# Kernel optimization log

Hardware: AMD Instinct MI355X
Metric: run time of the kernel (lower is better)

The kernel has to match this reference:

```python
import jax, jax.numpy as jnp
import numpy as np

B, T, H, F, Z = 4096, 16, 256, 256, 128   # batch, time_step, hidden, feature_dims, z_dims
P, PREV = 10, 5                           # predicted_visit, previous_visit


def _dense(x, W, b):
    return jax.nn.relu(x @ W + b)


def _forward(h_i, input_t, noise_post, noise_prior, W_lstm, U_lstm, b_lstm,
             W1, b1, W2, b2, W3, b3, W4, b4, W5, b5, W6, b6, W7, b7, W8, b8, W9, b9,
             alpha, beta, base):
    batch = h_i.shape[0]
    c = jnp.zeros((batch, H), h_i.dtype)
    h = jnp.zeros((batch, H), h_i.dtype)
    z_j = jnp.zeros((batch, Z), h_i.dtype)
    y_prev = jnp.zeros((batch, F), h_i.dtype)
    ys, m_post, lv_post, m_prior, lv_prior, z_post, z_prior, probs = ([] for _ in range(8))
    for j in range(P):  # sequential decode loop (true recurrence)
        cti = PREV + j
        # --- Hawkes intensity over growing history window [0, cti) ---
        ct = input_t[:, cti:cti + 1]                 # [B,1] current event time
        tb = input_t[:, :cti]                        # [B,cti] times before t
        tk = jnp.sum(jnp.exp(beta * (tb - ct)), axis=1, keepdims=True)   # [B,1]
        lam = base + alpha * tk                      # conditional intensity [B,1]
        last = input_t[:, cti - 1:cti]               # [B,1]
        td3 = jnp.sum(jnp.exp(beta * (tb - last)), axis=1, keepdims=True)
        prob = lam * jnp.exp((last - ct) * base + (alpha / beta) * (tk - td3))  # [B,1]
        # --- LSTM cell step (keras gate order i,f,c,o) ---
        x = jnp.concatenate([z_j, h_i, y_prev], axis=1)   # [B, Z+H+F]
        gates = x @ W_lstm + h @ U_lstm + b_lstm
        gi, gf, gg, go = jnp.split(gates, 4, axis=1)
        c = jax.nn.sigmoid(gf) * c + jax.nn.sigmoid(gi) * jnp.tanh(gg)
        h_raw = jax.nn.sigmoid(go) * jnp.tanh(c)          # LSTM output == new hidden
        h = lam * h_raw                                   # Hawkes-modulated hidden carried forward
        # --- emission ---
        y = _dense(_dense(_dense(h_raw, W1, b1), W2, b2), W3, b3)
        # --- inference (posterior) network ---
        hz = _dense(jnp.concatenate([h_i, h_raw, y, y_prev], axis=1), W4, b4)
        mean_j = _dense(hz, W5, b5)
        logv_j = _dense(hz, W6, b6)
        zj = mean_j + noise_post[j] * jnp.sqrt(jnp.exp(logv_j))
        # --- prior network ---
        hz_p = _dense(jnp.concatenate([h_i, h_raw, y_prev], axis=1), W7, b7)
        mean_p = _dense(hz_p, W8, b8)
        logv_p = _dense(hz_p, W9, b9)
        zp = mean_p + noise_prior[j] * jnp.sqrt(jnp.exp(logv_p))
        ys.append(y); m_post.append(mean_j); lv_post.append(logv_j)
        m_prior.append(mean_p); lv_prior.append(logv_p)
        z_post.append(zj); z_prior.append(zp); probs.append(prob)
        z_j, y_prev = zj, y
    return (jnp.stack(ys, 1),        # fake_input       [B,P,F]
            jnp.stack(m_post, 1),    # mean_all_post    [B,P,Z]
            jnp.stack(lv_post, 1),   # log_var_all_post [B,P,Z]
            jnp.stack(m_prior, 1),   # mean_all_prior   [B,P,Z]
            jnp.stack(lv_prior, 1),  # log_var_all_prior[B,P,Z]
            jnp.stack(z_post, 0),    # posterior z_all  [P,B,Z]
            jnp.stack(z_prior, 0),   # prior z_all      [P,B,Z]
            jnp.concatenate(probs, 0))  # time probs [P*B,1]


def setup_inputs() -> dict:
    key = jax.random.key(0)
    ks = jax.random.split(key, 20)
    u = lambda k, shape: jax.random.uniform(k, shape, jnp.float32, -0.05, 0.05)
    in_dim = Z + H + F
    return {
        "h_i": jax.random.normal(ks[0], (B, H), jnp.float32),
        "input_t": jnp.cumsum(jax.random.uniform(ks[1], (B, T), jnp.float32), axis=1),  # increasing event times
        "noise_post": jax.random.normal(ks[2], (P, B, Z), jnp.float32),
        "noise_prior": jax.random.normal(ks[3], (P, B, Z), jnp.float32),
        "W_lstm": u(ks[4], (in_dim, 4 * H)),
        "U_lstm": u(ks[5], (H, 4 * H)),
        "b_lstm": jnp.zeros((4 * H,), jnp.float32),
        "W1": u(ks[6], (H, F)), "b1": jnp.zeros((F,), jnp.float32),
        "W2": u(ks[7], (F, F)), "b2": jnp.zeros((F,), jnp.float32),
        "W3": u(ks[8], (F, F)), "b3": jnp.zeros((F,), jnp.float32),
        "W4": u(ks[9], (2 * H + 2 * F, Z)), "b4": jnp.zeros((Z,), jnp.float32),
        "W5": u(ks[10], (Z, Z)), "b5": jnp.zeros((Z,), jnp.float32),
        "W6": u(ks[11], (Z, Z)), "b6": jnp.zeros((Z,), jnp.float32),
        "W7": u(ks[12], (2 * H + F, Z)), "b7": jnp.zeros((Z,), jnp.float32),
        "W8": u(ks[13], (Z, Z)), "b8": jnp.zeros((Z,), jnp.float32),
        "W9": u(ks[14], (Z, Z)), "b9": jnp.zeros((Z,), jnp.float32),
        "alpha": u(ks[15], (1, 1)),
        "beta": u(ks[16], (1, 1)) + 0.1,   # keep away from 0 (alpha/beta division)
        "base": u(ks[17], (1, 1)),
    }


def reference(h_i, input_t, noise_post, noise_prior, W_lstm, U_lstm, b_lstm,
              W1, b1, W2, b2, W3, b3, W4, b4, W5, b5, W6, b6, W7, b7, W8, b8, W9, b9,
              alpha, beta, base):
    return _forward(h_i, input_t, noise_post, noise_prior, W_lstm, U_lstm, b_lstm,
                    W1, b1, W2, b2, W3, b3, W4, b4, W5, b5, W6, b6, W7, b7, W8, b8, W9, b9,
                    alpha, beta, base)
```

## Files before the change

### kernel.cpp

```cpp
#include <hip/hip_runtime.h>
#include <hip/hip_bf16.h>
#include <cstdint>
#include <cstddef>

#define DEVI __device__ __forceinline__

typedef __bf16 v8bf __attribute__((ext_vector_type(8)));
typedef float  v4f  __attribute__((ext_vector_type(4)));
using u16 = unsigned short;

constexpr int kB = 4096, kT = 16, kH = 256, kF = 256, kZ = 128, kP = 10, kPrev = 5;
constexpr int kRows = 16;
constexpr int kThreads = 1024;

constexpr size_t OFF_WzT = 0;
constexpr size_t OFF_WhT = OFF_WzT + (size_t)1024 * 128;
constexpr size_t OFF_WyT = OFF_WhT + (size_t)1024 * 256;
constexpr size_t OFF_UT  = OFF_WyT + (size_t)1024 * 256;
constexpr size_t OFF_W1T = OFF_UT  + (size_t)1024 * 256;
constexpr size_t OFF_W2T = OFF_W1T + (size_t)256 * 256;
constexpr size_t OFF_W3T = OFF_W2T + (size_t)256 * 256;
constexpr size_t OFF_W4T = OFF_W3T + (size_t)256 * 256;
constexpr size_t OFF_W5T = OFF_W4T + (size_t)128 * 1024;
constexpr size_t OFF_W6T = OFF_W5T + (size_t)128 * 128;
constexpr size_t OFF_W7T = OFF_W6T + (size_t)128 * 128;
constexpr size_t OFF_W8T = OFF_W7T + (size_t)128 * 768;
constexpr size_t OFF_W9T = OFF_W8T + (size_t)128 * 128;
constexpr size_t OFF_WEND= OFF_W9T + (size_t)128 * 128;

constexpr size_t O_YS   = 0;
constexpr size_t O_MPO  = O_YS   + (size_t)kB * kP * kF;
constexpr size_t O_LVPO = O_MPO  + (size_t)kB * kP * kZ;
constexpr size_t O_MPR  = O_LVPO + (size_t)kB * kP * kZ;
constexpr size_t O_LVPR = O_MPR  + (size_t)kB * kP * kZ;
constexpr size_t O_ZPO  = O_LVPR + (size_t)kB * kP * kZ;
constexpr size_t O_ZPR  = O_ZPO  + (size_t)kP * kB * kZ;
constexpr size_t O_PROB = O_ZPR  + (size_t)kP * kB * kZ;

DEVI float bf2f(u16 u) { return __uint_as_float(((unsigned)u) << 16); }
DEVI u16 f2bf(float f) {
    unsigned x = __float_as_uint(f);
    return (u16)((x + 0x7fffu + ((x >> 16) & 1u)) >> 16);
}
DEVI unsigned pk2(float lo, float hi) { return (unsigned)f2bf(lo) | ((unsigned)f2bf(hi) << 16); }
DEVI float upk(unsigned u, int hi) { return __uint_as_float(hi ? (u & 0xffff0000u) : (u << 16)); }
DEVI float sigf(float x) { x = fminf(fmaxf(x, -40.f), 40.f); return 1.f / (1.f + __expf(-x)); }
DEVI float tanhf_(float x) {
    x = fminf(fmaxf(x, -15.f), 15.f);
    float e = __expf(2.f * x);
    return (e - 1.f) / (e + 1.f);
}
DEVI v8bf ld8(const u16* p) { return *(const v8bf*)p; }
DEVI void nts(float v, float* p) { __builtin_nontemporal_store(v, p); }
DEVI float ntl(const float* p) { return __builtin_nontemporal_load(p); }

template <int NTL>
DEVI void zacc(v4f (&a)[NTL]) {
#pragma unroll
    for (int t = 0; t < NTL; ++t) a[t] = v4f{0, 0, 0, 0};
}

template <int K, int NTL, class NFN>
DEVI void gemm_acc(v4f (&acc)[NTL], const u16* A, int astr,
                   const u16* __restrict__ WT, int wtK, int wtOff,
                   NFN nf, int ln, int q) {
    const u16* A0 = A + ln * astr + q * 8;
    const u16* B0 = WT + (size_t)ln * wtK + (size_t)wtOff + q * 8;
#pragma unroll
    for (int k0 = 0; k0 < K; k0 += 32) {
        v8bf b[NTL];
#pragma unroll
        for (int t = 0; t < NTL; ++t)
            b[t] = ld8(B0 + (size_t)nf(t) * wtK + k0);
        v8bf a0 = ld8(A0 + k0);
#pragma unroll
        for (int t = 0; t < NTL; ++t)
            acc[t] = __builtin_amdgcn_mfma_f32_16x16x32_bf16(a0, b[t], acc[t], 0, 0, 0);
    }
}

DEVI void gemm2_128(v4f& aA, v4f& aB, const u16* A, int astr,
                    const u16* __restrict__ BA, const u16* __restrict__ BB,
                    int ln, int q) {
    const u16* A0 = A + ln * astr + q * 8;
    const u16* pa = BA + (size_t)ln * 128 + q * 8;
    const u16* pb = BB + (size_t)ln * 128 + q * 8;
#pragma unroll
    for (int k0 = 0; k0 < 128; k0 += 32) {
        v8bf b1 = ld8(pa + k0);
        v8bf b2 = ld8(pb + k0);
        v8bf av = ld8(A0 + k0);
        aA = __builtin_amdgcn_mfma_f32_16x16x32_bf16(av, b1, aA, 0, 0, 0);
        aB = __builtin_amdgcn_mfma_f32_16x16x32_bf16(av, b2, aB, 0, 0, 0);
    }
}

template <int NTL, class NFN>
DEVI void epi_relu(v4f (&acc)[NTL], const float (&bias)[NTL],
                   u16* s_dst, int dstr, NFN nf, int ln, int q) {
#pragma unroll
    for (int t = 0; t < NTL; ++t)
#pragma unroll
        for (int r = 0; r < 4; ++r) {
            int rl = q * 4 + r, n = nf(t) + ln;
            s_dst[rl * dstr + n] = f2bf(fmaxf(acc[t][r] + bias[t], 0.f));
        }
}

__global__ void transpose_w(const float* __restrict__ Wl, const float* __restrict__ U,
                            const float* __restrict__ W1, const float* __restrict__ W2,
                            const float* __restrict__ W3, const float* __restrict__ W4,
                            const float* __restrict__ W5, const float* __restrict__ W6,
                            const float* __restrict__ W7, const float* __restrict__ W8,
                            const float* __restrict__ W9, u16* __restrict__ ws) {
    size_t e = (size_t)blockIdx.x * blockDim.x + threadIdx.x;
    auto tp = [&](size_t eo, size_t dst, const float* src, int K, int srcN, int rowOff) {
        size_t n = eo / (size_t)K;
        size_t k = eo - n * (size_t)K;
        ws[dst + eo] = f2bf(src[(size_t)(rowOff + k) * srcN + n]);
    };
    if      (e < OFF_WhT) tp(e - OFF_WzT, OFF_WzT, Wl, 128, 1024, 0);
    else if (e < OFF_WyT) tp(e - OFF_WhT, OFF_WhT, Wl, 256, 1024, 128);
    else if (e < OFF_UT)  tp(e - OFF_WyT, OFF_WyT, Wl, 256, 1024, 384);
    else if (e < OFF_W1T) tp(e - OFF_UT,  OFF_UT,  U,  256, 1024, 0);
    else if (e < OFF_W2T) tp(e - OFF_W1T, OFF_W1T, W1, 256, 256, 0);
    else if (e < OFF_W3T) tp(e - OFF_W2T, OFF_W2T, W2, 256, 256, 0);
    else if (e < OFF_W4T) tp(e - OFF_W3T, OFF_W3T, W3, 256, 256, 0);
    else if (e < OFF_W5T) tp(e - OFF_W4T, OFF_W4T, W4, 1024, 128, 0);
    else if (e < OFF_W6T) tp(e - OFF_W5T, OFF_W5T, W5, 128, 128, 0);
    else if (e < OFF_W7T) tp(e - OFF_W6T, OFF_W6T, W6, 128, 128, 0);
    else if (e < OFF_W8T) tp(e - OFF_W7T, OFF_W7T, W7, 768, 128, 0);
    else if (e < OFF_W9T) tp(e - OFF_W8T, OFF_W8T, W8, 128, 128, 0);
    else if (e < OFF_WEND)tp(e - OFF_W9T, OFF_W9T, W9, 128, 128, 0);
}

__global__ __launch_bounds__(1024, 1) void fused_vrnn(
    const float* __restrict__ g_hi, const float* __restrict__ g_t,
    const float* __restrict__ g_npo, const float* __restrict__ g_npr,
    const float* __restrict__ b_lstm, const float* __restrict__ b1,
    const float* __restrict__ b2, const float* __restrict__ b3,
    const float* __restrict__ b4, const float* __restrict__ b5,
    const float* __restrict__ b6, const float* __restrict__ b7,
    const float* __restrict__ b8, const float* __restrict__ b9,
    const float* __restrict__ g_alpha, const float* __restrict__ g_beta,
    const float* __restrict__ g_base,
    const u16* __restrict__ ws, float* __restrict__ out) {
    __shared__ __align__(16) u16 s_h[kRows][kH + 8];
    __shared__ __align__(16) u16 s_zj[kRows][kZ + 8];
    __shared__ __align__(16) u16 s_yp[2][kRows][kF + 8];
    __shared__ __align__(16) u16 s_hraw[kRows][kH + 8];
    __shared__ __align__(16) u16 s_t1[kRows][kF + 8];
    __shared__ __align__(16) u16 s_t2[kRows][kF + 8];
    __shared__ __align__(16) u16 s_hz[kRows][kZ + 8];
    __shared__ __align__(16) u16 s_hzp[kRows][kZ + 8];
    __shared__ float s_lam[kP][kRows];

    const int tid = threadIdx.x;
    const int w = tid >> 6, lane = tid & 63, ln = lane & 15, q = lane >> 4;
    const int wl = w & 7;
    const bool lo = (w < 8);
    const int r0 = blockIdx.x * kRows;

    for (int i = tid; i < kRows * (kH + 8); i += kThreads) (&s_h[0][0])[i] = 0;
    for (int i = tid; i < kRows * (kZ + 8); i += kThreads) (&s_zj[0][0])[i] = 0;
    for (int i = tid; i < 2 * kRows * (kF + 8); i += kThreads) (&s_yp[0][0][0])[i] = 0;
    for (int i = tid; i < kRows * kH; i += kThreads) {
        int r = i >> 8, c = i & (kH - 1);
        s_hraw[r][c] = f2bf(g_hi[(size_t)(r0 + r) * kH + c]);
    }

    if (tid < kRows) {
        const float alpha = g_alpha[0], beta = g_beta[0], base = g_base[0];
        float tv[kT];
#pragma unroll
        for (int i = 0; i < kT; ++i) tv[i] = g_t[(size_t)(r0 + tid) * kT + i];
#pragma unroll 1
        for (int j = 0; j < kP; ++j) {
            int cti = kPrev + j;
            float ct = tv[cti], last = tv[cti - 1];
            float tk = 0.f, td3 = 0.f;
            for (int i = 0; i < cti; ++i) {
                tk += __expf(beta * (tv[i] - ct));
                td3 += __expf(beta * (tv[i] - last));
            }
            float lam = base + alpha * tk;
            float prob = lam * __expf((last - ct) * base + (alpha / beta) * (tk - td3));
            s_lam[j][tid] = lam;
            nts(prob, &out[O_PROB + (size_t)j * kB + (size_t)(r0 + tid)]);
        }
    }

    auto nfg  = [&](int t) { return (t << 8) + (w << 4); };
    auto nf12 = [&](int t) { return (w + (t << 3)) << 4; };
    auto nf3  = [&](int)   { return w << 4; };
    auto nfh  = [&](int)   { return wl << 4; };

    float rbl[4];
#pragma unroll
    for (int g = 0; g < 4; ++g) rbl[g] = b_lstm[(g << 8) + (w << 4) + ln];
    float rb1[2] = {0.f, 0.f}, rb2[2] = {0.f, 0.f};
    if (lo) {
#pragma unroll
        for (int t = 0; t < 2; ++t) {
            rb1[t] = b1[nf12(t) + ln];
            rb2[t] = b2[nf12(t) + ln];
        }
    }
    const float rb3v = b3[(w << 4) + ln];
    const int nhl = (wl << 4) + ln;
    float rb4 = 0.f, rb5 = 0.f, rb6 = 0.f, rb7 = 0.f, rb8 = 0.f, rb9 = 0.f;
    if (lo) { rb5 = b5[nhl]; rb6 = b6[nhl]; }
    else    { rb4 = b4[nhl]; rb7 = b7[nhl]; rb8 = b8[nhl]; rb9 = b9[nhl]; }

    __syncthreads();

    unsigned ghi_p[4][2];
    unsigned h4i_p[2] = {0, 0};
    unsigned h7i_p[2] = {0, 0};
    {
        v4f acc[4]; zacc(acc);
        gemm_acc<256, 4>(acc, &s_hraw[0][0], kH + 8, ws + OFF_WhT, 256, 0, nfg, ln, q);
#pragma unroll
        for (int t = 0; t < 4; ++t) {
            ghi_p[t][0] = pk2(acc[t][0], acc[t][1]);
            ghi_p[t][1] = pk2(acc[t][2], acc[t][3]);
        }
    }
    if (!lo) {
        v4f a[1]; zacc(a);
        gemm_acc<256, 1>(a, &s_hraw[0][0], kH + 8, ws + OFF_W4T, 1024, 0, nfh, ln, q);
        h4i_p[0] = pk2(a[0][0], a[0][1]);
        h4i_p[1] = pk2(a[0][2], a[0][3]);
        v4f b[1]; zacc(b);
        gemm_acc<256, 1>(b, &s_hraw[0][0], kH + 8, ws + OFF_W7T, 768, 0, nfh, ln, q);
        h7i_p[0] = pk2(b[0][0], b[0][1]);
        h7i_p[1] = pk2(b[0][2], b[0][3]);
    }
    __syncthreads();

    float c_st[4] = {0.f, 0.f, 0.f, 0.f};

#pragma unroll 1
    for (int j = 0; j < kP; ++j) {
        const int cur = j & 1, nxt = cur ^ 1;

        {
            v4f acc[4]; zacc(acc);
            gemm_acc<128, 4>(acc, &s_zj[0][0], kZ + 8, ws + OFF_WzT, 128, 0, nfg, ln, q);
            gemm_acc<256, 4>(acc, &s_yp[cur][0][0], kF + 8, ws + OFF_WyT, 256, 0, nfg, ln, q);
            gemm_acc<256, 4>(acc, &s_h[0][0], kH + 8, ws + OFF_UT, 256, 0, nfg, ln, q);
            __syncthreads();
            const int nc = (w << 4) + ln;
#pragma unroll
            for (int r = 0; r < 4; ++r) {
                const int rl = q * 4 + r;
                float gi = acc[0][r] + upk(ghi_p[0][r >> 1], r & 1) + rbl[0];
                float gf = acc[1][r] + upk(ghi_p[1][r >> 1], r & 1) + rbl[1];
                float gg = acc[2][r] + upk(ghi_p[2][r >> 1], r & 1) + rbl[2];
                float go = acc[3][r] + upk(ghi_p[3][r >> 1], r & 1) + rbl[3];
                float cs = c_st[r];
                cs = sigf(gf) * cs + sigf(gi) * tanhf_(gg);
                float hr = sigf(go) * tanhf_(cs);
                c_st[r] = cs;
                float lamv = s_lam[j][rl];
                s_hraw[rl][nc] = f2bf(hr);
                s_h[rl][nc] = f2bf(lamv * hr);
            }
        }
        __syncthreads();

        v4f a4[1]; zacc(a4);

        if (lo) {
            v4f a1[2]; zacc(a1);
            gemm_acc<256, 2>(a1, &s_hraw[0][0], kH + 8, ws + OFF_W1T, 256, 0, nf12, ln, q);
            epi_relu<2>(a1, rb1, &s_t1[0][0], kF + 8, nf12, ln, q);
        } else {
            v4f a7[1]; zacc(a7);
            gemm_acc<256, 1>(a7, &s_hraw[0][0], kH + 8, ws + OFF_W7T, 768, 256, nfh, ln, q);
            gemm_acc<256, 1>(a7, &s_yp[cur][0][0], kF + 8, ws + OFF_W7T, 768, 512, nfh, ln, q);
#pragma unroll
            for (int r = 0; r < 4; ++r) {
                float v = a7[0][r] + upk(h7i_p[r >> 1], r & 1) + rb7;
                s_hzp[q * 4 + r][nhl] = f2bf(fmaxf(v, 0.f));
            }
        }
        __syncthreads();

        if (lo) {
            v4f a2[2]; zacc(a2);
            gemm_acc<256, 2>(a2, &s_t1[0][0], kF + 8, ws + OFF_W2T, 256, 0, nf12, ln, q);
            epi_relu<2>(a2, rb2, &s_t2[0][0], kF + 8, nf12, ln, q);
        } else {
            gemm_acc<256, 1>(a4, &s_hraw[0][0], kH + 8, ws + OFF_W4T, 1024, 256, nfh, ln, q);
            gemm_acc<256, 1>(a4, &s_yp[cur][0][0], kF + 8, ws + OFF_W4T, 1024, 768, nfh, ln, q);
        }
        __syncthreads();

        {
            v4f a3[1]; zacc(a3);
            v4f a8 = v4f{0, 0, 0, 0}, a9 = v4f{0, 0, 0, 0};
            gemm_acc<256, 1>(a3, &s_t2[0][0], kF + 8, ws + OFF_W3T, 256, 0, nf3, ln, q);
            if (!lo)
                gemm2_128(a8, a9, &s_hzp[0][0], kZ + 8,
                          ws + OFF_W8T + (size_t)(wl << 4) * 128,
                          ws + OFF_W9T + (size_t)(wl << 4) * 128, ln, q);
            const int n3 = (w << 4) + ln;
#pragma unroll
            for (int r = 0; r < 4; ++r) {
                int rl = q * 4 + r;
                size_t grow = (size_t)(r0 + rl);
                float yv = fmaxf(a3[0][r] + rb3v, 0.f);
                s_yp[nxt][rl][n3] = f2bf(yv);
                nts(yv, &out[O_YS + (grow * kP + j) * kF + n3]);
            }
            if (!lo) {
#pragma unroll
                for (int r = 0; r < 4; ++r) {
                    int rl = q * 4 + r;
                    size_t grow = (size_t)(r0 + rl);
                    float mp = fmaxf(a8[r] + rb8, 0.f);
                    float lp = fmaxf(a9[r] + rb9, 0.f);
                    nts(mp, &out[O_MPR + (grow * kP + j) * kZ + nhl]);
                    nts(lp, &out[O_LVPR + (grow * kP + j) * kZ + nhl]);
                    float nz = ntl(&g_npr[((size_t)j * kB + grow) * kZ + nhl]);
                    nts(mp + nz * __expf(0.5f * lp),
                        &out[O_ZPR + ((size_t)j * kB + grow) * kZ + nhl]);
                }
            }
        }
        __syncthreads();

        if (!lo) {
            gemm_acc<256, 1>(a4, &s_yp[nxt][0][0], kF + 8, ws + OFF_W4T, 1024, 512, nfh, ln, q);
#pragma unroll
            for (int r = 0; r < 4; ++r) {
                float v = a4[0][r] + upk(h4i_p[r >> 1], r & 1) + rb4;
                s_hz[q * 4 + r][nhl] = f2bf(fmaxf(v, 0.f));
            }
        }
        __syncthreads();

        if (lo) {
            v4f a5 = v4f{0, 0, 0, 0}, a6 = v4f{0, 0, 0, 0};
            gemm2_128(a5, a6, &s_hz[0][0], kZ + 8,
                      ws + OFF_W5T + (size_t)(w << 4) * 128,
                      ws + OFF_W6T + (size_t)(w << 4) * 128, ln, q);
#pragma unroll
            for (int r = 0; r < 4; ++r) {
                int rl = q * 4 + r;
                size_t grow = (size_t)(r0 + rl);
                float mn = fmaxf(a5[r] + rb5, 0.f);
                float lv = fmaxf(a6[r] + rb6, 0.f);
                nts(mn, &out[O_MPO + (grow * kP + j) * kZ + nhl]);
                nts(lv, &out[O_LVPO + (grow * kP + j) * kZ + nhl]);
                float nz = ntl(&g_npo[((size_t)j * kB + grow) * kZ + nhl]);
                float zj = mn + nz * __expf(0.5f * lv);
                s_zj[rl][nhl] = f2bf(zj);
                nts(zj, &out[O_ZPO + ((size_t)j * kB + grow) * kZ + nhl]);
            }
        }
        __syncthreads();
    }
}

extern "C" void kernel_launch(void* const* d_in, const int* in_sizes, int n_in,
                              void* d_out, int out_size, void* d_ws, size_t ws_size,
                              hipStream_t stream) {
    const float* hi  = (const float*)d_in[0];
    const float* it  = (const float*)d_in[1];
    const float* npo = (const float*)d_in[2];
    const float* npr = (const float*)d_in[3];
    const float* Wl  = (const float*)d_in[4];
    const float* U   = (const float*)d_in[5];
    const float* bl  = (const float*)d_in[6];
    const float* W1  = (const float*)d_in[7];
    const float* b1  = (const float*)d_in[8];
    const float* W2  = (const float*)d_in[9];
    const float* b2  = (const float*)d_in[10];
    const float* W3  = (const float*)d_in[11];
    const float* b3  = (const float*)d_in[12];
    const float* W4  = (const float*)d_in[13];
    const float* b4  = (const float*)d_in[14];
    const float* W5  = (const float*)d_in[15];
    const float* b5  = (const float*)d_in[16];
    const float* W6  = (const float*)d_in[17];
    const float* b6  = (const float*)d_in[18];
    const float* W7  = (const float*)d_in[19];
    const float* b7  = (const float*)d_in[20];
    const float* W8  = (const float*)d_in[21];
    const float* b8  = (const float*)d_in[22];
    const float* W9  = (const float*)d_in[23];
    const float* b9  = (const float*)d_in[24];
    const float* al  = (const float*)d_in[25];
    const float* be  = (const float*)d_in[26];
    const float* ba  = (const float*)d_in[27];
    u16* ws   = (u16*)d_ws;
    float* out = (float*)d_out;

    const unsigned tblocks = (unsigned)((OFF_WEND + 255) / 256);
    transpose_w<<<dim3(tblocks), dim3(256), 0, stream>>>(Wl, U, W1, W2, W3, W4, W5, W6, W7, W8, W9, ws);
    fused_vrnn<<<dim3(kB / kRows), dim3(kThreads), 0, stream>>>(
        hi, it, npo, npr, bl, b1, b2, b3, b4, b5, b6, b7, b8, b9, al, be, ba, ws, out);
}
```

Baseline: 1.373 ms.

## Pre-swizzle weights into MFMA fragment order for contiguous per-wave loads

The weight transpose kernel now writes each bf16 weight matrix in 16x32 MFMA B-fragment blocks, so every wave's lane reads 8 contiguous elements and one whole fragment is a contiguous 1 KB chunk. The gemm helpers index by tile and k-block instead of strided rows, which turns scattered row-strided global loads into fully coalesced ones. The launch bounds also change from a minimum of one block per CU to amdgpu_waves_per_eu(4,4), which alters the register budget the compiler is given. Fragment indexing must match the MFMA operand layout exactly or the results will be wrong.

```diff
diff --git a/kernel.cpp b/kernel.cpp
--- a/kernel.cpp
+++ b/kernel.cpp
@@ -60,19 +60,19 @@
     for (int t = 0; t < NTL; ++t) a[t] = v4f{0, 0, 0, 0};
 }
 
-template <int K, int NTL, class NFN>
+template <int KB, int NTL, class TFN>
 DEVI void gemm_acc(v4f (&acc)[NTL], const u16* A, int astr,
-                   const u16* __restrict__ WT, int wtK, int wtOff,
-                   NFN nf, int ln, int q) {
+                   const u16* __restrict__ WP, int nkbFull, int kb0,
+                   TFN tf, int ln, int q, int lane) {
     const u16* A0 = A + ln * astr + q * 8;
-    const u16* B0 = WT + (size_t)ln * wtK + (size_t)wtOff + q * 8;
-#pragma unroll
-    for (int k0 = 0; k0 < K; k0 += 32) {
+    const u16* B0 = WP + (size_t)lane * 8;
+#pragma unroll
+    for (int kb = 0; kb < KB; ++kb) {
         v8bf b[NTL];
 #pragma unroll
         for (int t = 0; t < NTL; ++t)
-            b[t] = ld8(B0 + (size_t)nf(t) * wtK + k0);
-        v8bf a0 = ld8(A0 + k0);
+            b[t] = ld8(B0 + ((size_t)tf(t) * nkbFull + kb0 + kb) * 512);
+        v8bf a0 = ld8(A0 + kb * 32);
 #pragma unroll
         for (int t = 0; t < NTL; ++t)
             acc[t] = __builtin_amdgcn_mfma_f32_16x16x32_bf16(a0, b[t], acc[t], 0, 0, 0);
@@ -81,28 +81,28 @@
 
 DEVI void gemm2_128(v4f& aA, v4f& aB, const u16* A, int astr,
                     const u16* __restrict__ BA, const u16* __restrict__ BB,
-                    int ln, int q) {
+                    int tile, int ln, int q, int lane) {
     const u16* A0 = A + ln * astr + q * 8;
-    const u16* pa = BA + (size_t)ln * 128 + q * 8;
-    const u16* pb = BB + (size_t)ln * 128 + q * 8;
-#pragma unroll
-    for (int k0 = 0; k0 < 128; k0 += 32) {
-        v8bf b1 = ld8(pa + k0);
-        v8bf b2 = ld8(pb + k0);
-        v8bf av = ld8(A0 + k0);
+    const u16* pa = BA + (size_t)tile * 4 * 512 + (size_t)lane * 8;
+    const u16* pb = BB + (size_t)tile * 4 * 512 + (size_t)lane * 8;
+#pragma unroll
+    for (int kb = 0; kb < 4; ++kb) {
+        v8bf b1 = ld8(pa + kb * 512);
+        v8bf b2 = ld8(pb + kb * 512);
+        v8bf av = ld8(A0 + kb * 32);
         aA = __builtin_amdgcn_mfma_f32_16x16x32_bf16(av, b1, aA, 0, 0, 0);
         aB = __builtin_amdgcn_mfma_f32_16x16x32_bf16(av, b2, aB, 0, 0, 0);
     }
 }
 
-template <int NTL, class NFN>
+template <int NTL, class TFN>
 DEVI void epi_relu(v4f (&acc)[NTL], const float (&bias)[NTL],
-                   u16* s_dst, int dstr, NFN nf, int ln, int q) {
+                   u16* s_dst, int dstr, TFN tf, int ln, int q) {
 #pragma unroll
     for (int t = 0; t < NTL; ++t)
 #pragma unroll
         for (int r = 0; r < 4; ++r) {
-            int rl = q * 4 + r, n = nf(t) + ln;
+            int rl = q * 4 + r, n = (tf(t) << 4) + ln;
             s_dst[rl * dstr + n] = f2bf(fmaxf(acc[t][r] + bias[t], 0.f));
         }
 }
@@ -114,10 +114,17 @@
                             const float* __restrict__ W7, const float* __restrict__ W8,
                             const float* __restrict__ W9, u16* __restrict__ ws) {
     size_t e = (size_t)blockIdx.x * blockDim.x + threadIdx.x;
-    auto tp = [&](size_t eo, size_t dst, const float* src, int K, int srcN, int rowOff) {
-        size_t n = eo / (size_t)K;
-        size_t k = eo - n * (size_t)K;
-        ws[dst + eo] = f2bf(src[(size_t)(rowOff + k) * srcN + n]);
+    auto tp = [&](size_t eo, size_t dst, const float* src, int Kfull, int srcN, int rowOff) {
+        size_t chunk = eo >> 3, j = eo & 7;
+        int lane = (int)(chunk & 63);
+        size_t blk = chunk >> 6;
+        int nkb = Kfull >> 5;
+        int kb = (int)(blk % (size_t)nkb);
+        size_t n0 = blk / (size_t)nkb;
+        int ln = lane & 15, qq = lane >> 4;
+        size_t n = n0 * 16 + (size_t)ln;
+        size_t k = (size_t)kb * 32 + (size_t)qq * 8 + j;
+        ws[dst + eo] = f2bf(src[((size_t)rowOff + k) * srcN + n]);
     };
     if      (e < OFF_WhT) tp(e - OFF_WzT, OFF_WzT, Wl, 128, 1024, 0);
     else if (e < OFF_WyT) tp(e - OFF_WhT, OFF_WhT, Wl, 256, 1024, 128);
@@ -134,7 +141,8 @@
     else if (e < OFF_WEND)tp(e - OFF_W9T, OFF_W9T, W9, 128, 128, 0);
 }
 
-__global__ __launch_bounds__(1024, 1) void fused_vrnn(
+__global__ __launch_bounds__(1024)
+__attribute__((amdgpu_waves_per_eu(4, 4))) void fused_vrnn(
     const float* __restrict__ g_hi, const float* __restrict__ g_t,
     const float* __restrict__ g_npo, const float* __restrict__ g_npr,
     const float* __restrict__ b_lstm, const float* __restrict__ b1,
@@ -190,10 +198,10 @@
         }
     }
 
-    auto nfg  = [&](int t) { return (t << 8) + (w << 4); };
-    auto nf12 = [&](int t) { return (w + (t << 3)) << 4; };
-    auto nf3  = [&](int)   { return w << 4; };
-    auto nfh  = [&](int)   { return wl << 4; };
+    auto tg  = [&](int t) { return (t << 4) + w; };
+    auto t12 = [&](int t) { return w + (t << 3); };
+    auto t3  = [&](int)   { return w; };
+    auto th  = [&](int)   { return wl; };
 
     float rbl[4];
 #pragma unroll
@@ -202,8 +210,8 @@
     if (lo) {
 #pragma unroll
         for (int t = 0; t < 2; ++t) {
-            rb1[t] = b1[nf12(t) + ln];
-            rb2[t] = b2[nf12(t) + ln];
+            rb1[t] = b1[(t12(t) << 4) + ln];
+            rb2[t] = b2[(t12(t) << 4) + ln];
         }
     }
     const float rb3v = b3[(w << 4) + ln];
@@ -219,7 +227,7 @@
     unsigned h7i_p[2] = {0, 0};
     {
         v4f acc[4]; zacc(acc);
-        gemm_acc<256, 4>(acc, &s_hraw[0][0], kH + 8, ws + OFF_WhT, 256, 0, nfg, ln, q);
+        gemm_acc<8, 4>(acc, &s_hraw[0][0], kH + 8, ws + OFF_WhT, 8, 0, tg, ln, q, lane);
 #pragma unroll
         for (int t = 0; t < 4; ++t) {
             ghi_p[t][0] = pk2(acc[t][0], acc[t][1]);
@@ -228,11 +236,11 @@
     }
     if (!lo) {
         v4f a[1]; zacc(a);
-        gemm_acc<256, 1>(a, &s_hraw[0][0], kH + 8, ws + OFF_W4T, 1024, 0, nfh, ln, q);
+        gemm_acc<8, 1>(a, &s_hraw[0][0], kH + 8, ws + OFF_W4T, 32, 0, th, ln, q, lane);
         h4i_p[0] = pk2(a[0][0], a[0][1]);
         h4i_p[1] = pk2(a[0][2], a[0][3]);
         v4f b[1]; zacc(b);
-        gemm_acc<256, 1>(b, &s_hraw[0][0], kH + 8, ws + OFF_W7T, 768, 0, nfh, ln, q);
+        gemm_acc<8, 1>(b, &s_hraw[0][0], kH + 8, ws + OFF_W7T, 24, 0, th, ln, q, lane);
         h7i_p[0] = pk2(b[0][0], b[0][1]);
         h7i_p[1] = pk2(b[0][2], b[0][3]);
     }
@@ -246,9 +254,9 @@
 
         {
             v4f acc[4]; zacc(acc);
-            gemm_acc<128, 4>(acc, &s_zj[0][0], kZ + 8, ws + OFF_WzT, 128, 0, nfg, ln, q);
-            gemm_acc<256, 4>(acc, &s_yp[cur][0][0], kF + 8, ws + OFF_WyT, 256, 0, nfg, ln, q);
-            gemm_acc<256, 4>(acc, &s_h[0][0], kH + 8, ws + OFF_UT, 256, 0, nfg, ln, q);
+            gemm_acc<4, 4>(acc, &s_zj[0][0], kZ + 8, ws + OFF_WzT, 4, 0, tg, ln, q, lane);
+            gemm_acc<8, 4>(acc, &s_yp[cur][0][0], kF + 8, ws + OFF_WyT, 8, 0, tg, ln, q, lane);
+            gemm_acc<8, 4>(acc, &s_h[0][0], kH + 8, ws + OFF_UT, 8, 0, tg, ln, q, lane);
             __syncthreads();
             const int nc = (w << 4) + ln;
 #pragma unroll
@@ -273,12 +281,12 @@
 
         if (lo) {
             v4f a1[2]; zacc(a1);
-            gemm_acc<256, 2>(a1, &s_hraw[0][0], kH + 8, ws + OFF_W1T, 256, 0, nf12, ln, q);
-            epi_relu<2>(a1, rb1, &s_t1[0][0], kF + 8, nf12, ln, q);
+            gemm_acc<8, 2>(a1, &s_hraw[0][0], kH + 8, ws + OFF_W1T, 8, 0, t12, ln, q, lane);
+            epi_relu<2>(a1, rb1, &s_t1[0][0], kF + 8, t12, ln, q);
         } else {
             v4f a7[1]; zacc(a7);
-            gemm_acc<256, 1>(a7, &s_hraw[0][0], kH + 8, ws + OFF_W7T, 768, 256, nfh, ln, q);
-            gemm_acc<256, 1>(a7, &s_yp[cur][0][0], kF + 8, ws + OFF_W7T, 768, 512, nfh, ln, q);
+            gemm_acc<8, 1>(a7, &s_hraw[0][0], kH + 8, ws + OFF_W7T, 24, 8, th, ln, q, lane);
+            gemm_acc<8, 1>(a7, &s_yp[cur][0][0], kF + 8, ws + OFF_W7T, 24, 16, th, ln, q, lane);
 #pragma unroll
             for (int r = 0; r < 4; ++r) {
                 float v = a7[0][r] + upk(h7i_p[r >> 1], r & 1) + rb7;
@@ -289,22 +297,21 @@
 
         if (lo) {
             v4f a2[2]; zacc(a2);
-            gemm_acc<256, 2>(a2, &s_t1[0][0], kF + 8, ws + OFF_W2T, 256, 0, nf12, ln, q);
-            epi_relu<2>(a2, rb2, &s_t2[0][0], kF + 8, nf12, ln, q);
+            gemm_acc<8, 2>(a2, &s_t1[0][0], kF + 8, ws + OFF_W2T, 8, 0, t12, ln, q, lane);
+            epi_relu<2>(a2, rb2, &s_t2[0][0], kF + 8, t12, ln, q);
         } else {
-            gemm_acc<256, 1>(a4, &s_hraw[0][0], kH + 8, ws + OFF_W4T, 1024, 256, nfh, ln, q);
-            gemm_acc<256, 1>(a4, &s_yp[cur][0][0], kF + 8, ws + OFF_W4T, 1024, 768, nfh, ln, q);
+            gemm_acc<8, 1>(a4, &s_hraw[0][0], kH + 8, ws + OFF_W4T, 32, 8, th, ln, q, lane);
+            gemm_acc<8, 1>(a4, &s_yp[cur][0][0], kF + 8, ws + OFF_W4T, 32, 24, th, ln, q, lane);
         }
         __syncthreads();
 
         {
             v4f a3[1]; zacc(a3);
             v4f a8 = v4f{0, 0, 0, 0}, a9 = v4f{0, 0, 0, 0};
-            gemm_acc<256, 1>(a3, &s_t2[0][0], kF + 8, ws + OFF_W3T, 256, 0, nf3, ln, q);
+            gemm_acc<8, 1>(a3, &s_t2[0][0], kF + 8, ws + OFF_W3T, 8, 0, t3, ln, q, lane);
             if (!lo)
                 gemm2_128(a8, a9, &s_hzp[0][0], kZ + 8,
-                          ws + OFF_W8T + (size_t)(wl << 4) * 128,
-                          ws + OFF_W9T + (size_t)(wl << 4) * 128, ln, q);
+                          ws + OFF_W8T, ws + OFF_W9T, wl, ln, q, lane);
             const int n3 = (w << 4) + ln;
 #pragma unroll
             for (int r = 0; r < 4; ++r) {
@@ -332,7 +339,7 @@
         __syncthreads();
 
         if (!lo) {
-            gemm_acc<256, 1>(a4, &s_yp[nxt][0][0], kF + 8, ws + OFF_W4T, 1024, 512, nfh, ln, q);
+            gemm_acc<8, 1>(a4, &s_yp[nxt][0][0], kF + 8, ws + OFF_W4T, 32, 16, th, ln, q, lane);
 #pragma unroll
             for (int r = 0; r < 4; ++r) {
                 float v = a4[0][r] + upk(h4i_p[r >> 1], r & 1) + rb4;
@@ -344,8 +351,7 @@
         if (lo) {
             v4f a5 = v4f{0, 0, 0, 0}, a6 = v4f{0, 0, 0, 0};
             gemm2_128(a5, a6, &s_hz[0][0], kZ + 8,
-                      ws + OFF_W5T + (size_t)(w << 4) * 128,
-                      ws + OFF_W6T + (size_t)(w << 4) * 128, ln, q);
+                      ws + OFF_W5T, ws + OFF_W6T, w, ln, q, lane);
 #pragma unroll
             for (int r = 0; r < 4; ++r) {
                 int rl = q * 4 + r;
```

After: 1.496 ms. 1.09x slower.
